# Performance work log

Measured on AMD Instinct MI355X. Metric: run time of the kernel, lower is better.

The kernel has to match this reference:

```python
import jax, jax.numpy as jnp
import numpy as np

N, C, T, V = 16, 64, 300, 25
NH, DK, DV = 4, 64, 64
DKH = DK // NH
DVH = DV // NH
EPS = 1e-5


def rel_to_abs(x):
    # x: (B, Nh, L, 2L-1) relative logits -> (B, Nh, L, L) absolute, via skew trick
    B, Nh, L, _ = x.shape
    x = jnp.pad(x, ((0, 0), (0, 0), (0, 0), (0, 1)))          # (B,Nh,L,2L)
    flat = x.reshape(B, Nh, L * 2 * L)
    flat = jnp.pad(flat, ((0, 0), (0, 0), (0, L - 1)))
    final = flat.reshape(B, Nh, L + 1, 2 * L - 1)
    return final[:, :, :L, L - 1:]


def setup_inputs() -> dict:
    key = jax.random.key(0)
    ks = jax.random.split(key, 12)
    return {
        "x": jax.random.normal(ks[0], (N, C, T, V), jnp.float32),
        "dbn_g": jax.random.normal(ks[1], (C * V,), jnp.float32),
        "dbn_b": jax.random.normal(ks[2], (C * V,), jnp.float32),
        "dbn_m": jax.random.normal(ks[3], (C * V,), jnp.float32) * 0.1,
        "dbn_v": jax.random.uniform(ks[4], (C * V,), jnp.float32, 0.5, 1.5),
        "qkv_w": jax.random.normal(ks[5], (2 * DK + DV, C), jnp.float32) * 0.05,
        "qkv_b": jax.random.normal(ks[6], (2 * DK + DV,), jnp.float32) * 0.05,
        "key_rel": jax.random.normal(ks[7], (2 * T - 1, DKH), jnp.float32),
        "attn_w": jax.random.normal(ks[8], (DV, DV), jnp.float32) * 0.05,
        "attn_b": jax.random.normal(ks[9], (DV,), jnp.float32) * 0.05,
        "bn_g": jax.random.normal(ks[10], (DV,), jnp.float32),
        "bn_b": jax.random.normal(ks[11], (DV,), jnp.float32),
        "bn_m": jnp.zeros((DV,), jnp.float32),
        "bn_v": jnp.ones((DV,), jnp.float32),
    }


def reference(x, dbn_g, dbn_b, dbn_m, dbn_v, qkv_w, qkv_b, key_rel,
              attn_w, attn_b, bn_g, bn_b, bn_m, bn_v):
    x_sum = x  # (N,C,T,V)
    # data_bn: BatchNorm1d (eval) over C*V channels on (N, C*V, T)
    xp = x.transpose(0, 1, 3, 2).reshape(N, C * V, T)
    xp = (xp - dbn_m[None, :, None]) * jax.lax.rsqrt(dbn_v + EPS)[None, :, None] \
         * dbn_g[None, :, None] + dbn_b[None, :, None]
    xn = xp.reshape(N, C, V, T).transpose(0, 1, 3, 2)          # (N,C,T,V)
    # per-joint temporal sequences: (N*V, C, T)
    xa = xn.transpose(0, 3, 1, 2).reshape(N * V, C, T)
    # 1x1 qkv conv
    qkv = jnp.einsum('oc,bct->bot', qkv_w, xa) + qkv_b[None, :, None]
    B = N * V
    q = qkv[:, :DK].reshape(B, NH, DKH, T) * (DKH ** -0.5)
    k = qkv[:, DK:2 * DK].reshape(B, NH, DKH, T)
    v = qkv[:, 2 * DK:].reshape(B, NH, DVH, T)
    logits = jnp.einsum('bhdt,bhds->bhts', q, k)               # (B,NH,T,T)
    rel = jnp.einsum('bhdt,md->bhtm', q, key_rel)              # (B,NH,T,2T-1)
    logits = logits + rel_to_abs(rel)
    w = jax.nn.softmax(logits, axis=-1)
    attn = jnp.einsum('bhts,bhds->bhtd', w, v)                 # (B,NH,T,DVH)
    attn = attn.transpose(0, 1, 3, 2).reshape(B, DV, T)        # combine heads
    attn = jnp.einsum('od,bdt->bot', attn_w, attn) + attn_b[None, :, None]
    out = attn.reshape(N, V, DV, T).transpose(0, 2, 3, 1)      # (N,DV,T,V)
    res = out + x_sum                                          # skip (down is None)
    res = (res - bn_m[None, :, None, None]) * jax.lax.rsqrt(bn_v + EPS)[None, :, None, None] \
          * bn_g[None, :, None, None] + bn_b[None, :, None, None]
    return jax.nn.relu(res)
```

## Files before the change

kernel.cpp:

```cpp
#include <hip/hip_runtime.h>
#include <hip/hip_bf16.h>
#include <cstddef>

#define NN 16
#define CC 64
#define TT 300
#define VV 25
#define NHH 4
#define DKHH 16
#define BB (NN * VV)
#define EPS 1e-5f
#define LOG2E 1.4426950408889634f

#define WS_QK    0
#define WS_V     7680000
#define WS_AH    11571200
#define WS_REL   15462400
#define WS_AWF   15472896
#define WS_AOFF  15474944
#define WS_SCO   15475008
#define WS_WFRAG 15475072
#define WS_QB2   15481216
#define WS_SCSH  15481408

typedef __attribute__((ext_vector_type(8))) short short8;
typedef __attribute__((ext_vector_type(4))) float float4v;

union U8 { short8 v; unsigned int w[4]; };

__device__ __forceinline__ unsigned int pk2(float a, float b) {
#if __has_builtin(__builtin_amdgcn_cvt_pk_bf16_f32)
    typedef __attribute__((ext_vector_type(2))) __bf16 bf2;
    union { bf2 v; unsigned u; } c;
    c.v = __builtin_amdgcn_cvt_pk_bf16_f32(a, b);
    return c.u;
#else
    union { float f; unsigned u; } x, y;
    x.f = a; y.f = b;
    unsigned ua = x.u + 0x7FFFu + ((x.u >> 16) & 1u);
    unsigned ub = y.u + 0x7FFFu + ((y.u >> 16) & 1u);
    return (ua >> 16) | (ub & 0xFFFF0000u);
#endif
}

__device__ __forceinline__ float ex2(float x) {
#if __has_builtin(__builtin_amdgcn_exp2f)
    return __builtin_amdgcn_exp2f(x);
#else
    return exp2f(x);
#endif
}

__device__ __forceinline__ float rcpf_(float x) {
#if __has_builtin(__builtin_amdgcn_rcpf)
    return __builtin_amdgcn_rcpf(x);
#else
    return 1.f / x;
#endif
}

__global__ __launch_bounds__(256) void k_pre(
    const float* __restrict__ dbn_g, const float* __restrict__ dbn_b,
    const float* __restrict__ dbn_m, const float* __restrict__ dbn_v,
    const float* __restrict__ qkv_w, const float* __restrict__ qkv_b,
    const float* __restrict__ key_rel,
    const float* __restrict__ attn_w, const float* __restrict__ attn_b,
    const float* __restrict__ bn_g, const float* __restrict__ bn_b,
    const float* __restrict__ bn_m, const float* __restrict__ bn_v,
    unsigned* __restrict__ W)
{
    const int jid = blockIdx.x * 256 + threadIdx.x;
    if (jid < 2624) {
        const int k = jid >> 6, lane = jid & 63, col = lane & 15, quad = lane >> 4;
        const int mt = k - 1, m = mt * 16 + col;
        const bool ok = (quad < 2) && (mt >= 0) && (m < 2 * TT - 1);
        unsigned w[4];
        #pragma unroll
        for (int j2 = 0; j2 < 4; ++j2) {
            const int c = quad * 8 + 2 * j2;
            const float v0 = ok ? key_rel[m * 16 + c] : 0.f;
            const float v1 = ok ? key_rel[m * 16 + c + 1] : 0.f;
            w[j2] = pk2(v0, v1);
        }
        *(uint4*)&W[WS_REL + k * 256 + lane * 4] = make_uint4(w[0], w[1], w[2], w[3]);
    } else if (jid < 3136) {
        const int e = jid - 2624;
        const int ot = e >> 7, ch = (e >> 6) & 1, lane = e & 63;
        const int col = lane & 15, quad = lane >> 4;
        const int o = ot * 16 + col;
        const float sc = bn_g[o] * rsqrtf(bn_v[o] + EPS);
        unsigned w[4];
        #pragma unroll
        for (int j2 = 0; j2 < 4; ++j2) {
            const int c = ch * 32 + quad * 8 + 2 * j2;
            w[j2] = pk2(attn_w[o * 64 + c] * sc, attn_w[o * 64 + c + 1] * sc);
        }
        *(uint4*)&W[WS_AWF + (ot * 2 + ch) * 256 + lane * 4] = make_uint4(w[0], w[1], w[2], w[3]);
    } else if (jid < 3200) {
        const int o = jid - 3136;
        const float sc = bn_g[o] * rsqrtf(bn_v[o] + EPS);
        ((float*)(W + WS_AOFF))[o] = attn_b[o] * sc + bn_b[o] - bn_m[o] * sc;
    } else if (jid < 3264) {
        const int o = jid - 3200;
        ((float*)(W + WS_SCO))[o] = bn_g[o] * rsqrtf(bn_v[o] + EPS);
    } else if (jid < 4800) {
        const int e = jid - 3264;
        const int ot = e >> 7, ch = (e >> 6) & 1, lane = e & 63;
        const int col = lane & 15, quad = lane >> 4;
        const int o = ot * 16 + col;
        const float qs = (o < 64) ? 0.25f * LOG2E : 1.f;
        unsigned w[4];
        #pragma unroll
        for (int j2 = 0; j2 < 4; ++j2) {
            const int c = ch * 32 + quad * 8 + 2 * j2;
            w[j2] = pk2(qkv_w[o * 64 + c] * qs, qkv_w[o * 64 + c + 1] * qs);
        }
        *(uint4*)&W[WS_WFRAG + (ot * 2 + ch) * 256 + lane * 4] = make_uint4(w[0], w[1], w[2], w[3]);
    } else if (jid < 4992) {
        const int o = jid - 4800;
        ((float*)(W + WS_QB2))[o] = qkv_b[o] * ((o < 64) ? 0.25f * LOG2E : 1.f);
    } else if (jid < 6592) {
        const int e = jid - 4992;
        const float sc = dbn_g[e] * rsqrtf(dbn_v[e] + EPS);
        const float sh = dbn_b[e] - dbn_m[e] * sc;
        ((float2*)(W + WS_SCSH))[e] = make_float2(sc, sh);
    }
}

__global__ __launch_bounds__(1024) void k_qkv(
        const float* __restrict__ x, unsigned* __restrict__ W)
{
    const int tt = blockIdx.x, n = blockIdx.y, t0 = tt * 16;
    const int tid = threadIdx.x;
    const unsigned* wfrag = W + WS_WFRAG;
    const float* qb2 = (const float*)(W + WS_QB2);
    unsigned* qk_p = W + WS_QK;
    unsigned* v_p  = W + WS_V;

    __shared__ unsigned afrag[25 * 516];
    __shared__ float2 sls[1600];

    for (int i = tid; i < 1600; i += 1024)
        sls[i] = ((const float2*)(W + WS_SCSH))[i];
    __syncthreads();

    for (int i = tid; i < 3200; i += 1024) {
        const int f4 = i % 100, cp = i / 100;
        const int c0 = cp * 2;
        float4 xa = make_float4(0.f, 0.f, 0.f, 0.f);
        float4 xb = make_float4(0.f, 0.f, 0.f, 0.f);
        if (tt < 18 || f4 < 75) {
            const float* p = x + (size_t)(n * 64 + c0) * 7500 + tt * 400 + f4 * 4;
            xa = *(const float4*)p;
            xb = *(const float4*)(p + 7500);
        }
        const int ch = cp >> 4, qd = (cp >> 2) & 3, j2 = cp & 3;
        const float ea[4] = {xa.x, xa.y, xa.z, xa.w};
        const float eb[4] = {xb.x, xb.y, xb.z, xb.w};
        #pragma unroll
        for (int e = 0; e < 4; ++e) {
            const int flat = f4 * 4 + e;
            const int tl = (flat * 5243) >> 17;
            const int v  = flat - 25 * tl;
            const float2 s0 = sls[c0 * 25 + v];
            const float2 s1 = sls[c0 * 25 + 25 + v];
            const float a0 = fmaf(ea[e], s0.x, s0.y);
            const float a1 = fmaf(eb[e], s1.x, s1.y);
            afrag[v * 516 + (ch * 64 + qd * 16 + tl) * 4 + j2] = pk2(a0, a1);
        }
    }
    __syncthreads();

    const int wvv = tid >> 6, lane = tid & 63, col = lane & 15, quad = lane >> 4;
    const int otg = wvv >> 2, vq = wvv & 3;
    const int vlo = (vq == 0) ? 0 : (1 + 6 * vq);
    const int vhi = 7 + 6 * vq;
    const float4v zero4 = {0.f, 0.f, 0.f, 0.f};
    const bool tvalid = (t0 + 4 * quad + 3 < TT);

    U8 bf[3][2]; float qb_l[3];
    #pragma unroll
    for (int i = 0; i < 3; ++i) {
        const int ot = 3 * otg + i;
        #pragma unroll
        for (int ch = 0; ch < 2; ++ch) {
            const uint4 u = *(const uint4*)&wfrag[(ot * 2 + ch) * 256 + lane * 4];
            bf[i][ch].w[0] = u.x; bf[i][ch].w[1] = u.y; bf[i][ch].w[2] = u.z; bf[i][ch].w[3] = u.w;
        }
        qb_l[i] = qb2[ot * 16 + col];
    }

    for (int v = vlo; v < vhi; ++v) {
        const int b = n * 25 + v;
        U8 a0, a1;
        { const uint4 u = *(const uint4*)&afrag[v * 516 + lane * 4];
          a0.w[0] = u.x; a0.w[1] = u.y; a0.w[2] = u.z; a0.w[3] = u.w; }
        { const uint4 u = *(const uint4*)&afrag[v * 516 + 256 + lane * 4];
          a1.w[0] = u.x; a1.w[1] = u.y; a1.w[2] = u.z; a1.w[3] = u.w; }
        #pragma unroll
        for (int i = 0; i < 3; ++i) {
            const int ot = 3 * otg + i;
            float4v acc = __builtin_amdgcn_mfma_f32_16x16x32_bf16(a0.v, bf[i][0].v, zero4, 0, 0, 0);
            acc = __builtin_amdgcn_mfma_f32_16x16x32_bf16(a1.v, bf[i][1].v, acc, 0, 0, 0);
            float val[4];
            #pragma unroll
            for (int r = 0; r < 4; ++r) val[r] = acc[r] + qb_l[i];
            if (ot < 8) {
                unsigned pk[4];
                #pragma unroll
                for (int r = 0; r < 4; ++r) {
                    const float p = __shfl_xor(val[r], 1);
                    pk[r] = pk2(val[r], p);
                }
                if (((col & 1) == 0) && tvalid) {
                    const int op = ot * 8 + (col >> 1);
                    *(uint4*)&qk_p[(size_t)(b * 64 + op) * TT + t0 + 4 * quad] =
                        make_uint4(pk[0], pk[1], pk[2], pk[3]);
                }
            } else {
                const int d = (ot - 8) * 16 + col;
                uint2 u;
                if (tvalid) { u.x = pk2(val[0], val[1]); u.y = pk2(val[2], val[3]); }
                else        { u.x = 0u; u.y = 0u; }
                *(uint2*)&v_p[(size_t)(b * 64 + d) * 152 + 8 * tt + 2 * quad] = u;
            }
        }
    }
}

__global__ __launch_bounds__(256, 4) void k_attn(unsigned* __restrict__ W)
{
    const int bh = blockIdx.x;
    const int b = bh >> 2, h = bh & 3;
    const int tid  = threadIdx.x;
    const int wave = tid >> 6, lane = tid & 63;
    const int col  = lane & 15, quad = lane >> 4;

    const unsigned* qk_p = W + WS_QK;
    const unsigned* v_p  = W + WS_V;
    unsigned* ah_p = W + WS_AH;
    const unsigned* relfrag = W + WS_REL;

    __shared__ unsigned kbuf[19 * 32 * 4];
    __shared__ unsigned vbuf[10 * 64 * 4];
    __shared__ float relbuf[4][16 * 68];

    for (int p = tid; p < 2432; p += 256) {
        const int c = p & 15, j2 = (p >> 4) & 3, qh = (p >> 6) & 1, st = p >> 7;
        kbuf[(st * 32 + qh * 16 + c) * 4 + j2] =
            qk_p[(size_t)(b * 64 + 32 + h * 8 + qh * 4 + j2) * TT + st * 16 + c];
    }
    for (int p = tid; p < 640; p += 256) {
        const int tq = p % 40, d = p / 40;
        const int off = (tq * 4 <= 148) ? tq * 4 : 144;
        const uint4 u = *(const uint4*)&v_p[(size_t)(b * 64 + h * 16 + d) * 152 + off];
        const int c = tq >> 2;
        const int l0 = (tq & 3) * 4;
        const unsigned uu[4] = {u.x, u.y, u.z, u.w};
        #pragma unroll
        for (int j = 0; j < 4; ++j) {
            const int local = l0 + j;
            const int q  = (local < 8) ? (local >> 1) : ((local - 8) >> 1);
            const int j2 = (local < 8) ? (local & 1) : (2 + (local & 1));
            vbuf[(c * 64 + q * 16 + d) * 4 + j2] = uu[j];
        }
    }
    __syncthreads();

    float* relw = &relbuf[wave][0];
    const float4v zero4 = {0.f, 0.f, 0.f, 0.f};
    U8 onef;
    onef.w[0] = onef.w[1] = onef.w[2] = onef.w[3] = 0x3F803F80u;

    for (int tt = wave; tt < 19; tt += 4) {
        const int t0 = tt * 16;

        U8 qf;
        if (quad < 2) {
            int t = t0 + col; if (t > TT - 1) t = TT - 1;
            const size_t rb = (size_t)(b * 64 + h * 8 + quad * 4) * TT + t;
            qf.w[0] = qk_p[rb];
            qf.w[1] = qk_p[rb + TT];
            qf.w[2] = qk_p[rb + 2 * TT];
            qf.w[3] = qk_p[rb + 3 * TT];
        } else {
            qf.w[0] = qf.w[1] = qf.w[2] = qf.w[3] = 0u;
        }

        auto rel_ld = [&](int mt) -> uint4 {
            return *(const uint4*)&relfrag[(mt + 1) * 256 + lane * 4];
        };
        auto rel_do = [&](int mt, uint4 u) {
            U8 kr; kr.w[0] = u.x; kr.w[1] = u.y; kr.w[2] = u.z; kr.w[3] = u.w;
            const float4v rc = __builtin_amdgcn_mfma_f32_16x16x32_bf16(
                                   kr.v, qf.v, zero4, 0, 0, 0);
            const int wbase = mt * 16 + 4 * quad + t0 + col + 21;
            float* rw = &relw[col * 68];
            rw[wbase & 63]       = rc[0];
            rw[(wbase + 1) & 63] = rc[1];
            rw[(wbase + 2) & 63] = rc[2];
            rw[(wbase + 3) & 63] = rc[3];
        };

        #pragma unroll
        for (int i = 0; i < 4; ++i) rel_do(17 - tt + i, rel_ld(17 - tt + i));
        uint4 ru0 = rel_ld(21 - tt), ru1 = rel_ld(22 - tt);

        float4v accPV = zero4;
        float4v accS  = zero4;

        #pragma unroll 3
        for (int c = 0; c < 9; ++c) {
            U8 kf0, kf1;
            if (quad < 2) {
                const uint4 u0 = *(const uint4*)&kbuf[((2 * c) * 32 + quad * 16 + col) * 4];
                const uint4 u1 = *(const uint4*)&kbuf[((2 * c + 1) * 32 + quad * 16 + col) * 4];
                kf0.w[0] = u0.x; kf0.w[1] = u0.y; kf0.w[2] = u0.z; kf0.w[3] = u0.w;
                kf1.w[0] = u1.x; kf1.w[1] = u1.y; kf1.w[2] = u1.z; kf1.w[3] = u1.w;
            } else {
                kf0.w[0] = kf0.w[1] = kf0.w[2] = kf0.w[3] = 0u;
                kf1.w[0] = kf1.w[1] = kf1.w[2] = kf1.w[3] = 0u;
            }
            const short8 vf = *(const short8*)&vbuf[(c * 64 + lane) * 4];

            const int rb0 = (32 * c + 4 * quad) & 63;
            const float4v rc0 = *(const float4v*)&relw[col * 68 + rb0];
            const float4v rc1 = *(const float4v*)&relw[col * 68 + ((rb0 + 16) & 63)];
            const float4v qk0 = __builtin_amdgcn_mfma_f32_16x16x32_bf16(kf0.v, qf.v, rc0, 0, 0, 0);
            const float4v qk1 = __builtin_amdgcn_mfma_f32_16x16x32_bf16(kf1.v, qf.v, rc1, 0, 0, 0);

            const float e0 = ex2(qk0[0]);
            const float e1 = ex2(qk0[1]);
            const float e2 = ex2(qk0[2]);
            const float e3 = ex2(qk0[3]);
            const float e4 = ex2(qk1[0]);
            const float e5 = ex2(qk1[1]);
            const float e6 = ex2(qk1[2]);
            const float e7 = ex2(qk1[3]);

            U8 pf;
            pf.w[0] = pk2(e0, e1);
            pf.w[1] = pk2(e2, e3);
            pf.w[2] = pk2(e4, e5);
            pf.w[3] = pk2(e6, e7);
            accPV = __builtin_amdgcn_mfma_f32_16x16x32_bf16(pf.v, vf, accPV, 0, 0, 0);
            accS  = __builtin_amdgcn_mfma_f32_16x16x32_bf16(pf.v, onef.v, accS, 0, 0, 0);

            rel_do(2 * c + 21 - tt, ru0);
            rel_do(2 * c + 22 - tt, ru1);
            if (c < 8) { ru0 = rel_ld(2 * c + 23 - tt); ru1 = rel_ld(2 * c + 24 - tt); }
        }

        {
            U8 kf0;
            if (quad < 2) {
                const uint4 u0 = *(const uint4*)&kbuf[(18 * 32 + quad * 16 + col) * 4];
                kf0.w[0] = u0.x; kf0.w[1] = u0.y; kf0.w[2] = u0.z; kf0.w[3] = u0.w;
            } else {
                kf0.w[0] = kf0.w[1] = kf0.w[2] = kf0.w[3] = 0u;
            }
            const int rb0 = (288 + 4 * quad) & 63;
            const float4v rc0 = *(const float4v*)&relw[col * 68 + rb0];
            const float4v qk0 = __builtin_amdgcn_mfma_f32_16x16x32_bf16(kf0.v, qf.v, rc0, 0, 0, 0);
            float e0 = ex2(qk0[0]);
            float e1 = ex2(qk0[1]);
            float e2 = ex2(qk0[2]);
            float e3 = ex2(qk0[3]);
            if (quad == 3) { e0 = e1 = e2 = e3 = 0.f; }
            U8 pf;
            pf.w[0] = pk2(e0, e1);
            pf.w[1] = pk2(e2, e3);
            pf.w[2] = 0u;
            pf.w[3] = 0u;
            const short8 vf = *(const short8*)&vbuf[(9 * 64 + lane) * 4];
            accPV = __builtin_amdgcn_mfma_f32_16x16x32_bf16(pf.v, vf, accPV, 0, 0, 0);
            accS  = __builtin_amdgcn_mfma_f32_16x16x32_bf16(pf.v, onef.v, accS, 0, 0, 0);
        }

        if (t0 + 4 * quad + 3 < TT) {
            uint2 u;
            u.x = pk2(accPV[0] * rcpf_(accS[0]), accPV[1] * rcpf_(accS[1]));
            u.y = pk2(accPV[2] * rcpf_(accS[2]), accPV[3] * rcpf_(accS[3]));
            *(uint2*)&ah_p[(size_t)(b * 64 + h * 16 + col) * 152 + 8 * tt + 2 * quad] = u;
        }
    }
}

__global__ __launch_bounds__(512) void k_out(
        const float* __restrict__ x, const unsigned* __restrict__ W,
        float* __restrict__ out)
{
    const int tt = blockIdx.x, n = blockIdx.y, tq = blockIdx.z;
    if (tt == 18 && tq == 3) return;
    const int t0q = tt * 16 + tq * 4;
    const int tid = threadIdx.x;
    const unsigned* ah_p = W + WS_AH;
    const unsigned* awfrag = W + WS_AWF;
    const float* aoff = (const float*)(W + WS_AOFF);
    const float* scO  = (const float*)(W + WS_SCO);

    __shared__ unsigned fbuf[4 * 1024];
    __shared__ float obuf[6400];

    for (int j = tid; j < 1600; j += 512) {
        const int o = j / 25, f4 = j - 25 * o;
        const float4 xv = *(const float4*)(x + (size_t)(n * 64 + o) * 7500 + t0q * 25 + f4 * 4);
        *(float4*)&obuf[o * 100 + f4 * 4] = xv;
    }
    for (int i = tid; i < 1600; i += 512) {
        const int tp2 = i & 1, pc = (i >> 1) & 31, v = i >> 6;
        const int b = n * 25 + v;
        const size_t r0 = (size_t)(b * 64 + 2 * pc) * 152 + tt * 8 + tq * 2 + tp2;
        const unsigned A = ah_p[r0], Bv = ah_p[r0 + 152];
        const unsigned ue = (A & 0xFFFFu) | (Bv << 16);
        const unsigned uo = (A >> 16) | (Bv & 0xFFFF0000u);
        const int vt = v >> 4, cv = v & 15, ch = pc >> 4, qd = (pc >> 2) & 3, j2 = pc & 3;
        const int xi = (vt * 2 + ch) * 256 + (qd * 16 + (cv ^ qd)) * 4 + j2;
        const int tl = 2 * tp2;
        fbuf[tl * 1024 + ((xi + 12 * tl) & 1023)]             = ue;
        fbuf[(tl + 1) * 1024 + ((xi + 12 * (tl + 1)) & 1023)] = uo;
    }
    __syncthreads();

    const int wv = tid >> 6, lane = tid & 63, col = lane & 15, quad = lane >> 4;
    const int ow = wv & 3, th = wv >> 2;
    const int o = ow * 16 + col;
    const float4v zero4 = {0.f, 0.f, 0.f, 0.f};

    U8 awf0, awf1;
    { const uint4 u = *(const uint4*)&awfrag[(ow * 2 + 0) * 256 + lane * 4];
      awf0.w[0] = u.x; awf0.w[1] = u.y; awf0.w[2] = u.z; awf0.w[3] = u.w; }
    { const uint4 u = *(const uint4*)&awfrag[(ow * 2 + 1) * 256 + lane * 4];
      awf1.w[0] = u.x; awf1.w[1] = u.y; awf1.w[2] = u.z; awf1.w[3] = u.w; }
    const float aoff_l = aoff[o], sc_l = scO[o];

    for (int tl = 2 * th; tl < 2 * th + 2; ++tl) {
        #pragma unroll
        for (int vt = 0; vt < 2; ++vt) {
            U8 a0, a1;
            { const int xb = (vt * 2 + 0) * 256 + (quad * 16 + (col ^ quad)) * 4;
              const uint4 u = *(const uint4*)&fbuf[tl * 1024 + ((xb + 12 * tl) & 1023)];
              a0.w[0] = u.x; a0.w[1] = u.y; a0.w[2] = u.z; a0.w[3] = u.w; }
            { const int xb = (vt * 2 + 1) * 256 + (quad * 16 + (col ^ quad)) * 4;
              const uint4 u = *(const uint4*)&fbuf[tl * 1024 + ((xb + 12 * tl) & 1023)];
              a1.w[0] = u.x; a1.w[1] = u.y; a1.w[2] = u.z; a1.w[3] = u.w; }
            float4v acc = __builtin_amdgcn_mfma_f32_16x16x32_bf16(a0.v, awf0.v, zero4, 0, 0, 0);
            acc = __builtin_amdgcn_mfma_f32_16x16x32_bf16(a1.v, awf1.v, acc, 0, 0, 0);
            #pragma unroll
            for (int r = 0; r < 4; ++r) {
                const int v = vt * 16 + 4 * quad + r;
                if (v < 25) {
                    const int oi = o * 100 + tl * 25 + v;
                    obuf[oi] = fmaxf(fmaf(obuf[oi], sc_l, acc[r] + aoff_l), 0.f);
                }
            }
        }
    }
    __syncthreads();

    for (int j = tid; j < 1600; j += 512) {
        const int o2 = j / 25, f4 = j - 25 * o2;
        *(float4*)(out + (size_t)(n * 64 + o2) * 7500 + t0q * 25 + f4 * 4) =
            *(const float4*)&obuf[o2 * 100 + f4 * 4];
    }
}

extern "C" void kernel_launch(void* const* d_in, const int* in_sizes, int n_in,
                              void* d_out, int out_size, void* d_ws, size_t ws_size,
                              hipStream_t stream)
{
    const float* x       = (const float*)d_in[0];
    const float* dbn_g   = (const float*)d_in[1];
    const float* dbn_b   = (const float*)d_in[2];
    const float* dbn_m   = (const float*)d_in[3];
    const float* dbn_v   = (const float*)d_in[4];
    const float* qkv_w   = (const float*)d_in[5];
    const float* qkv_b   = (const float*)d_in[6];
    const float* key_rel = (const float*)d_in[7];
    const float* attn_w  = (const float*)d_in[8];
    const float* attn_b  = (const float*)d_in[9];
    const float* bn_g    = (const float*)d_in[10];
    const float* bn_b    = (const float*)d_in[11];
    const float* bn_m    = (const float*)d_in[12];
    const float* bn_v    = (const float*)d_in[13];
    float* out = (float*)d_out;
    unsigned* W = (unsigned*)d_ws;

    k_pre<<<26, 256, 0, stream>>>(dbn_g, dbn_b, dbn_m, dbn_v, qkv_w, qkv_b,
                                  key_rel, attn_w, attn_b, bn_g, bn_b, bn_m,
                                  bn_v, W);
    k_qkv<<<dim3(19, 16), 1024, 0, stream>>>(x, W);
    k_attn<<<1600, 256, 0, stream>>>(W);
    k_out<<<dim3(19, 16, 4), 512, 0, stream>>>(x, W, out);
}
```

Baseline: 233.9 us.

## Store attention output time-major with channel pairs packed for vectorized loads

The attention kernel now shuffles neighbouring channels and packs them into bf16 pairs. It writes the intermediate attention buffer in a (b, t, channel-pair) layout instead of a channel-major one with time pairs. The output-projection kernel can then load each tile with uint4 loads and place them directly into its fragment buffer, dropping the scalar loads and the bit-unpacking. The producer pays for extra shuffles and scattered 4-byte stores from only half the lanes. The old guard on t < T is also removed, so padded time rows are now written, which relies on the buffer holding 304 rows.

New measurement: 213.8 us. 8.6% less time.

```diff
diff --git a/kernel.cpp b/kernel.cpp
--- a/kernel.cpp
+++ b/kernel.cpp
@@ -377,11 +377,22 @@
             accS  = __builtin_amdgcn_mfma_f32_16x16x32_bf16(pf.v, onef.v, accS, 0, 0, 0);
         }
 
-        if (t0 + 4 * quad + 3 < TT) {
-            uint2 u;
-            u.x = pk2(accPV[0] * rcpf_(accS[0]), accPV[1] * rcpf_(accS[1]));
-            u.y = pk2(accPV[2] * rcpf_(accS[2]), accPV[3] * rcpf_(accS[3]));
-            *(uint2*)&ah_p[(size_t)(b * 64 + h * 16 + col) * 152 + 8 * tt + 2 * quad] = u;
+        {
+            float val[4];
+            #pragma unroll
+            for (int r = 0; r < 4; ++r) val[r] = accPV[r] * rcpf_(accS[r]);
+            unsigned w[4];
+            #pragma unroll
+            for (int r = 0; r < 4; ++r) {
+                const float p = __shfl_xor(val[r], 1);
+                w[r] = pk2(val[r], p);
+            }
+            if ((col & 1) == 0) {
+                const int dp = h * 8 + (col >> 1);
+                unsigned* dst = ah_p + (size_t)(b * 304 + t0 + 4 * quad) * 32 + dp;
+                #pragma unroll
+                for (int r = 0; r < 4; ++r) dst[r * 32] = w[r];
+            }
         }
     }
 }
@@ -407,18 +418,14 @@
         const float4 xv = *(const float4*)(x + (size_t)(n * 64 + o) * 7500 + t0q * 25 + f4 * 4);
         *(float4*)&obuf[o * 100 + f4 * 4] = xv;
     }
-    for (int i = tid; i < 1600; i += 512) {
-        const int tp2 = i & 1, pc = (i >> 1) & 31, v = i >> 6;
+    for (int i = tid; i < 800; i += 512) {
+        const int dp4 = i & 7, g = i >> 3;
+        const int tl = g & 3, v = g >> 2;
         const int b = n * 25 + v;
-        const size_t r0 = (size_t)(b * 64 + 2 * pc) * 152 + tt * 8 + tq * 2 + tp2;
-        const unsigned A = ah_p[r0], Bv = ah_p[r0 + 152];
-        const unsigned ue = (A & 0xFFFFu) | (Bv << 16);
-        const unsigned uo = (A >> 16) | (Bv & 0xFFFF0000u);
-        const int vt = v >> 4, cv = v & 15, ch = pc >> 4, qd = (pc >> 2) & 3, j2 = pc & 3;
-        const int xi = (vt * 2 + ch) * 256 + (qd * 16 + (cv ^ qd)) * 4 + j2;
-        const int tl = 2 * tp2;
-        fbuf[tl * 1024 + ((xi + 12 * tl) & 1023)]             = ue;
-        fbuf[(tl + 1) * 1024 + ((xi + 12 * (tl + 1)) & 1023)] = uo;
+        const uint4 u = *(const uint4*)&ah_p[(size_t)(b * 304 + t0q + tl) * 32 + dp4 * 4];
+        const int vt = v >> 4, cv = v & 15, ch = dp4 >> 2, qd = dp4 & 3;
+        const int xi0 = (vt * 2 + ch) * 256 + (qd * 16 + (cv ^ qd)) * 4;
+        *(uint4*)&fbuf[tl * 1024 + ((xi0 + 12 * tl) & 1023)] = u;
     }
     __syncthreads();
 
```
